# Optimization experiments

Measured on AMD Instinct MI355X. Metric: run time of the kernel, lower is better.

## Reference

```python
import jax, jax.numpy as jnp
import numpy as np

BS, NV, D, DFF, E, H = 32, 512, 128, 512, 8, 8
EPS = 1e-5

def layernorm(x, g, b):
    m = x.mean(-1, keepdims=True)
    v = ((x - m) ** 2).mean(-1, keepdims=True)
    return (x - m) / jnp.sqrt(v + EPS) * g + b

def setup_inputs() -> dict:
    key = jax.random.key(0)
    ks = jax.random.split(key, 10)
    s = lambda k, shape: (jax.random.normal(k, shape, jnp.float32) * 0.02)
    return {
        "x": jax.random.normal(ks[0], (BS, NV, D), jnp.float32),
        "cls_emd": jax.random.normal(ks[1], (E, D), jnp.float32),
        "Wq": s(ks[2], (D, D)), "Wk": s(ks[3], (D, D)),
        "Wv": s(ks[4], (D, D)), "Wo": s(ks[5], (D, D)),
        "Wg": s(ks[6], (D, D)),
        "W1": s(ks[7], (E, DFF, 2 * D)), "b1": jnp.zeros((E, DFF), jnp.float32),
        "W2": s(ks[8], (E, D, DFF)), "b2": jnp.zeros((E, D), jnp.float32),
        "g1": jnp.ones((D,), jnp.float32), "be1": jnp.zeros((D,), jnp.float32),
        "g2": jnp.ones((D,), jnp.float32), "be2": jnp.zeros((D,), jnp.float32),
    }

def reference(x, cls_emd, Wq, Wk, Wv, Wo, Wg, W1, b1, W2, b2, g1, be1, g2, be2):
    bs, n, d = x.shape
    dh = d // H
    # --- full multi-head self-attention over the variate axis ---
    q = (x @ Wq).reshape(bs, n, H, dh)
    k = (x @ Wk).reshape(bs, n, H, dh)
    v = (x @ Wv).reshape(bs, n, H, dh)
    scores = jnp.einsum('bnhd,bmhd->bhnm', q, k) * (1.0 / np.sqrt(dh))
    attn = jax.nn.softmax(scores, axis=-1)            # [bs, H, n, n]
    new_x = jnp.einsum('bhnm,bmhd->bnhd', attn, v).reshape(bs, n, d) @ Wo
    # residual + norm1 (dropout = identity in eval)
    x = layernorm(x + new_x, g1, be1)
    # --- gating: per-variate scores over clusters [n_vars, n_clusters] ---
    gate_scores = jax.nn.softmax((x.mean(0) @ Wg) @ cls_emd.T, axis=-1)
    # --- MoE: expand tokens vs every cluster, concat, per-cluster expert MLP ---
    ncl = cls_emd.shape[0]
    y = jnp.broadcast_to(x[:, :, None, :], (bs, n, ncl, d))
    z = jnp.broadcast_to(cls_emd[None, None, :, :], (bs, n, ncl, d))
    yz_cat = jnp.concatenate([y, z], axis=-1)          # [bs, n, K, 2d]
    h = jax.nn.relu(jnp.einsum('bnkc,kfc->bnkf', yz_cat, W1) + b1)  # kernel_size=1 conv == matmul
    expert_out = jnp.einsum('bnkf,kdf->bnkd', h, W2) + b2           # [bs, n, K, d]
    y_r = jnp.einsum('nk,bnkd->bnd', gate_scores, expert_out)
    out = layernorm(x + y_r, g2, be2)
    return (out, attn, gate_scores)
```

## Files before the change

kernel.cpp:

```cpp
#include <hip/hip_runtime.h>
#include <hip/hip_bf16.h>
#include <math.h>

#define BS   32
#define NV   512
#define D    128
#define DFF  512
#define E    8
#define NH   8
#define DH   16
#define M_TOK (BS*NV)
#define EPS  1e-5f

typedef __hip_bfloat16 bf16;
typedef _Float16 f16;
using sh8   = __attribute__((ext_vector_type(8))) short;
using us4   = __attribute__((ext_vector_type(4))) unsigned short;
using h4    = __attribute__((ext_vector_type(4))) _Float16;
using h8    = __attribute__((ext_vector_type(8))) _Float16;
using f32x4 = __attribute__((ext_vector_type(4))) float;

__device__ __forceinline__ float b2f(bf16 v){ return __bfloat162float(v); }
__device__ __forceinline__ bf16  f2b(float v){ return __float2bfloat16(v); }
__device__ __forceinline__ unsigned short f2bu(float v){
    bf16 b = __float2bfloat16(v);
    return __builtin_bit_cast(unsigned short, b);
}

__device__ __forceinline__ void gload_lds16(const void* g, void* l){
    __builtin_amdgcn_global_load_lds(
        (const __attribute__((address_space(1))) unsigned int*)g,
        (__attribute__((address_space(3))) unsigned int*)l, 16, 0, 0);
}

#define PR0 4096
#define PR1 (PR0 + 262144)
#define PR2 (PR1 + 131072)
#define PR3 (PR2 + 524288)
#define PR4 (PR3 + 49152)
#define PR5 (PR4 + 16384)
#define PREP_ITEMS PR5
__global__ __launch_bounds__(256) void k_prep(
    const float* __restrict__ W1, const float* __restrict__ W2,
    const float* __restrict__ x,  const float* __restrict__ Wq,
    const float* __restrict__ Wk, const float* __restrict__ Wv,
    const float* __restrict__ Wo, const float* __restrict__ b1,
    const float* __restrict__ cls,
    bf16* __restrict__ W1b, bf16* __restrict__ W2b, f16* __restrict__ xh,
    f16* __restrict__ WTq, f16* __restrict__ WoT, float* __restrict__ b1eff)
{
    int tid = blockIdx.x*256 + threadIdx.x;
    if (tid < PR0){
        int e = tid >> 9, f = tid & 511;
        float acc = b1[e*DFF + f];
        const float* wrow = W1 + ((size_t)e*DFF + f)*(2*D) + D;
        #pragma unroll 8
        for (int c=0;c<D;++c) acc += cls[e*D+c] * wrow[c];
        b1eff[tid] = acc;
    } else if (tid < PR1){
        int i = (tid - PR0)*4;
        float4 vv = *(const float4*)(W1 + i);
        us4 o; o[0]=f2bu(vv.x); o[1]=f2bu(vv.y); o[2]=f2bu(vv.z); o[3]=f2bu(vv.w);
        *(us4*)(W1b + i) = o;
    } else if (tid < PR2){
        int i = (tid - PR1)*4;
        float4 vv = *(const float4*)(W2 + i);
        us4 o; o[0]=f2bu(vv.x); o[1]=f2bu(vv.y); o[2]=f2bu(vv.z); o[3]=f2bu(vv.w);
        *(us4*)(W2b + i) = o;
    } else if (tid < PR3){
        int i = (tid - PR2)*4;
        float4 vv = *(const float4*)(x + i);
        h4 o; o[0]=(f16)vv.x; o[1]=(f16)vv.y; o[2]=(f16)vv.z; o[3]=(f16)vv.w;
        *(h4*)(xh + i) = o;
    } else if (tid < PR4){
        int idx = tid - PR3;
        int c = idx>>7, kk = idx&127;
        int which = c>>7, col = c&127;
        const float* W = which==0?Wq:(which==1?Wk:Wv);
        WTq[idx] = (f16)W[kk*D + col];
    } else if (tid < PR5){
        int idx = tid - PR4;
        int c = idx>>7, kk = idx&127;
        WoT[idx] = (f16)Wo[kk*D + c];
    }
}

__global__ __launch_bounds__(512) void k_qkv_mfma(
    const f16* __restrict__ xh, const f16* __restrict__ WT,
    f16* __restrict__ q, f16* __restrict__ k, f16* __restrict__ v)
{
    __shared__ __align__(16) char smem[65536];
    char* Xl = smem;
    char* Wl = smem + 16384;
    int t = threadIdx.x;
    int w = t>>6, lane = t&63;
    int bm = blockIdx.x, nh = blockIdx.y;

    const f16* xsrc = xh + (size_t)bm*64*D;
    #pragma unroll
    for (int i=0;i<2;++i){
        int ci = i*512 + t;
        int row = ci>>4, c16 = (ci&15)^(row&7);
        gload_lds16(xsrc + row*D + c16*8, Xl + (size_t)(i*512 + w*64)*16);
    }
    const f16* wsrc = WT + (size_t)nh*192*D;
    #pragma unroll
    for (int i=0;i<6;++i){
        int ci = i*512 + t;
        int row = ci>>4, c16 = (ci&15)^(row&7);
        gload_lds16(wsrc + row*D + c16*8, Wl + (size_t)(i*512 + w*64)*16);
    }
    __syncthreads();

    int rblk = w>>1, ch = w&1;
    int rl = lane&15, g = lane>>4;

    h8 afr[4];
    #pragma unroll
    for (int kk=0;kk<4;++kk){
        int row = rblk*16 + rl;
        int bo = (row<<8) + (kk<<6) + (g<<4); bo ^= (row&7)<<4;
        afr[kk] = *(const h8*)(Xl + bo);
    }
    f32x4 acc[6];
    #pragma unroll
    for (int nt=0;nt<6;++nt) acc[nt] = (f32x4){0.f,0.f,0.f,0.f};
    #pragma unroll
    for (int nt=0; nt<6; ++nt){
        #pragma unroll
        for (int kk=0;kk<4;++kk){
            int row = ch*96 + nt*16 + rl;
            int bo = (row<<8)+(kk<<6)+(g<<4); bo ^= (row&7)<<4;
            h8 bfr = *(const h8*)(Wl + bo);
            acc[nt] = __builtin_amdgcn_mfma_f32_16x16x32_f16(afr[kk], bfr, acc[nt],0,0,0);
        }
    }
    #pragma unroll
    for (int nt=0;nt<6;++nt){
        int cidx = nh*192 + ch*96 + nt*16 + rl;
        int which = cidx>>7, hh=(cidx>>4)&7, d = cidx&15;
        f16* dst = which==0?q:(which==1?k:v);
        #pragma unroll
        for (int j=0;j<4;++j){
            int m = bm*64 + rblk*16 + g*4 + j;
            int b = m>>9, n = m&511;
            dst[(((size_t)(b*NH+hh))*NV + n)*DH + d] = (f16)acc[nt][j];
        }
    }
}

#define KSTRIDE 24
#define VSTRIDE 520
#define PSTRIDE 68
__global__ __launch_bounds__(256) void k_attn2(
    const f16* __restrict__ q, const f16* __restrict__ kin, const f16* __restrict__ vin,
    float* __restrict__ attn_out, f16* __restrict__ ctx)
{
    __shared__ f16  Kl[512*KSTRIDE];
    __shared__ f16  VT[16*VSTRIDE];
    __shared__ f16  pbh[4][16*PSTRIDE];

    int bh = blockIdx.x;
    int t  = threadIdx.x;
    const f16* kb = kin + (size_t)bh*NV*DH;
    const f16* vb = vin + (size_t)bh*NV*DH;

    {
        int r0 = t*2;
        #pragma unroll
        for (int rr=0; rr<2; ++rr){
            const uint4* src = (const uint4*)(kb + (size_t)(r0+rr)*DH);
            *((uint4*)(Kl + (r0+rr)*KSTRIDE))     = src[0];
            *((uint4*)(Kl + (r0+rr)*KSTRIDE + 8)) = src[1];
        }
        const unsigned short* v0s = (const unsigned short*)(vb + (size_t)r0*DH);
        const unsigned short* v1s = v0s + DH;
        #pragma unroll
        for (int d=0; d<DH; ++d){
            unsigned u = (unsigned)v0s[d] | ((unsigned)v1s[d] << 16);
            *((unsigned*)(VT + d*VSTRIDE + r0)) = u;
        }
    }
    __syncthreads();

    int wave = t >> 6, lane = t & 63;
    int ql = lane & 15, g = lane >> 4;
    int q0 = blockIdx.y*64 + wave*16;

    h4 qf = *(const h4*)(q + ((size_t)bh*NV + q0 + ql)*DH + 4*g);
    #pragma unroll
    for (int i=0;i<4;++i) qf[i] = qf[i] * (_Float16)0.36067376f;

    f32x4 S[32];
    #pragma unroll
    for (int tt=0; tt<32; ++tt){
        h4 kf = *(const h4*)(Kl + (tt*16 + ql)*KSTRIDE + 4*g);
        S[tt] = __builtin_amdgcn_mfma_f32_16x16x16f16(kf, qf, (f32x4){0.f,0.f,0.f,0.f}, 0,0,0);
    }

    float sum = 0.f;
    #pragma unroll
    for (int tt=0; tt<32; ++tt)
        #pragma unroll
        for (int j=0;j<4;++j){
            float p = exp2f(S[tt][j]);
            S[tt][j] = p; sum += p;
        }
    sum += __shfl_xor(sum, 16);
    sum += __shfl_xor(sum, 32);
    float inv = 1.f/sum;
    #pragma unroll
    for (int tt=0; tt<32; ++tt)
        #pragma unroll
        for (int j=0;j<4;++j) S[tt][j] *= inv;

    f32x4 o0 = (f32x4){0.f,0.f,0.f,0.f}, o1 = (f32x4){0.f,0.f,0.f,0.f};
    f16* pw = pbh[wave];
    float* attnbase = attn_out + ((size_t)bh*NV + q0)*NV;
    int col16 = lane & 15, qg = lane >> 4;
    #pragma unroll
    for (int c=0; c<8; ++c){
        #pragma unroll
        for (int tt2=0; tt2<4; ++tt2){
            int tt = c*4 + tt2;
            h4 pf;
            pf[0]=(f16)S[tt][0]; pf[1]=(f16)S[tt][1];
            pf[2]=(f16)S[tt][2]; pf[3]=(f16)S[tt][3];
            h4 vf = *(const h4*)(VT + ql*VSTRIDE + tt*16 + 4*g);
            if (tt&1) o1 = __builtin_amdgcn_mfma_f32_16x16x16f16(vf, pf, o1, 0,0,0);
            else      o0 = __builtin_amdgcn_mfma_f32_16x16x16f16(vf, pf, o0, 0,0,0);
            *(h4*)(pw + ql*PSTRIDE + tt2*16 + 4*g) = pf;
        }
        asm volatile("" ::: "memory");
        #pragma unroll
        for (int rr=0; rr<4; ++rr){
            int qq = rr*4 + qg;
            h4 hv = *(const h4*)(pw + qq*PSTRIDE + col16*4);
            f32x4 vv;
            vv[0]=(float)hv[0]; vv[1]=(float)hv[1];
            vv[2]=(float)hv[2]; vv[3]=(float)hv[3];
            __builtin_nontemporal_store(vv, (f32x4*)(attnbase + (size_t)qq*NV + c*64 + col16*4));
        }
        asm volatile("" ::: "memory");
    }
    f32x4 o = o0 + o1;
    int b = bh >> 3, h = bh & 7;
    f16* cb = ctx + ((size_t)(b*NV) + q0 + ql)*D + h*DH + 4*g;
    h4 oc; oc[0]=(f16)o[0]; oc[1]=(f16)o[1]; oc[2]=(f16)o[2]; oc[3]=(f16)o[3];
    *(h4*)cb = oc;
}

__global__ __launch_bounds__(512) void k_woln_mfma(
    const f16* __restrict__ ctx, const f16* __restrict__ WoT,
    const float* __restrict__ x, const float* __restrict__ g1, const float* __restrict__ be1,
    bf16* __restrict__ x1b, float* __restrict__ yacc)
{
    __shared__ __align__(16) char smem[49152];
    __shared__ float lnred[2][64][2];
    char* Cl = smem;
    char* Wl = smem + 16384;
    int t = threadIdx.x;
    int w = t>>6, lane = t&63;
    int bm = blockIdx.x;

    const f16* csrc = ctx + (size_t)bm*64*D;
    #pragma unroll
    for (int i=0;i<2;++i){
        int ci = i*512 + t;
        int row = ci>>4, c16 = (ci&15)^(row&7);
        gload_lds16(csrc + row*D + c16*8, Cl + (size_t)(i*512 + w*64)*16);
    }
    #pragma unroll
    for (int i=0;i<4;++i){
        int ci = i*512 + t;
        int row = ci>>4, c16 = (ci&15)^(row&7);
        gload_lds16(WoT + row*D + c16*8, Wl + (size_t)(i*512 + w*64)*16);
    }
    __syncthreads();

    int rblk = w>>1, ch = w&1;
    int rl = lane&15, g = lane>>4;

    h8 afr[4];
    #pragma unroll
    for (int kk=0;kk<4;++kk){
        int row = rblk*16 + rl;
        int bo = (row<<8) + (kk<<6) + (g<<4); bo ^= (row&7)<<4;
        afr[kk] = *(const h8*)(Cl + bo);
    }
    f32x4 acc[4];
    #pragma unroll
    for (int nt=0;nt<4;++nt) acc[nt] = (f32x4){0.f,0.f,0.f,0.f};
    #pragma unroll
    for (int nt=0; nt<4; ++nt){
        #pragma unroll
        for (int kk=0;kk<4;++kk){
            int row = ch*64 + nt*16 + rl;
            int bo = (row<<8)+(kk<<6)+(g<<4); bo ^= (row&7)<<4;
            h8 bfr = *(const h8*)(Wl + bo);
            acc[nt] = __builtin_amdgcn_mfma_f32_16x16x32_f16(afr[kk], bfr, acc[nt],0,0,0);
        }
    }

    float rowv[4][4];
    #pragma unroll
    for (int j=0;j<4;++j){
        int m = bm*64 + rblk*16 + g*4 + j;
        #pragma unroll
        for (int dt=0;dt<4;++dt){
            int d = ch*64 + dt*16 + rl;
            rowv[j][dt] = acc[dt][j] + x[(size_t)m*D + d];
        }
    }
    #pragma unroll
    for (int j=0;j<4;++j){
        float s  = rowv[j][0]+rowv[j][1]+rowv[j][2]+rowv[j][3];
        float s2 = rowv[j][0]*rowv[j][0]+rowv[j][1]*rowv[j][1]
                 + rowv[j][2]*rowv[j][2]+rowv[j][3]*rowv[j][3];
        #pragma unroll
        for (int o=1;o<16;o<<=1){ s += __shfl_xor(s,o); s2 += __shfl_xor(s2,o); }
        if (rl==0){
            int row = rblk*16 + g*4 + j;
            lnred[ch][row][0] = s;
            lnred[ch][row][1] = s2;
        }
    }
    __syncthreads();
    #pragma unroll
    for (int j=0;j<4;++j){
        int row = rblk*16 + g*4 + j;
        float S  = lnred[0][row][0] + lnred[1][row][0];
        float S2 = lnred[0][row][1] + lnred[1][row][1];
        float mean = S*(1.f/D);
        float var  = S2*(1.f/D) - mean*mean;
        float rs = rsqrtf(var + EPS);
        int m = bm*64 + row;
        #pragma unroll
        for (int dt=0;dt<4;++dt){
            int d = ch*64 + dt*16 + rl;
            float o1 = (rowv[j][dt]-mean)*rs*g1[d] + be1[d];
            x1b[(size_t)m*D + d] = f2b(o1);
            yacc[(size_t)m*D + d] = o1;
        }
    }
}

__global__ __launch_bounds__(128) void k_gate(
    const float* __restrict__ yacc, const float* __restrict__ Wg, const float* __restrict__ cls,
    float* __restrict__ gate, float* __restrict__ gate_out)
{
    __shared__ float xm[D];
    __shared__ float tt[D];
    __shared__ float se[E];
    int n = blockIdx.x, t = threadIdx.x;
    float s = 0.f;
    #pragma unroll
    for (int b=0;b<BS;++b) s += yacc[((size_t)b*NV + n)*D + t];
    xm[t] = s * (1.f/BS);
    __syncthreads();
    float a = 0.f;
    for (int c=0;c<D;++c) a += xm[c] * Wg[c*D + t];
    tt[t] = a;
    __syncthreads();
    if (t < E){
        float acc=0.f;
        for (int c=0;c<D;++c) acc += tt[c] * cls[t*D + c];
        se[t]=acc;
    }
    __syncthreads();
    if (t==0){
        float mx=se[0];
        for(int e=1;e<E;++e) mx=fmaxf(mx,se[e]);
        float sm=0.f; float p[E];
        for(int e=0;e<E;++e){ p[e]=__expf(se[e]-mx); sm+=p[e]; }
        float inv=1.f/sm;
        for(int e=0;e<E;++e){
            gate[n*E+e]     = p[e]*inv;
            gate_out[n*E+e] = p[e]*inv;
        }
    }
}

__global__ __launch_bounds__(512) void k_moe_fused(
    const bf16* __restrict__ x1b, const bf16* __restrict__ W1b, const bf16* __restrict__ W2b,
    const float* __restrict__ b1eff, const float* __restrict__ b2,
    const float* __restrict__ gate, const float* __restrict__ yacc,
    const float* __restrict__ g2, const float* __restrict__ be2,
    float* __restrict__ out)
{
    __shared__ __align__(16) char smem[147456];
    char* Hl = smem + 131072;
    float (*lnred)[64][2] = (float (*)[64][2])Hl;

    int t = threadIdx.x;
    int w = t >> 6, lane = t & 63;
    int rblk = w >> 1, c = w & 1;
    int rl = lane & 15, g = lane >> 4;
    int bm = blockIdx.x;

    sh8 afr[4];
    {
        const bf16* Ab = x1b + (size_t)(bm*64 + rblk*16 + rl)*D;
        #pragma unroll
        for (int kk=0;kk<4;++kk) afr[kk] = *(const sh8*)(Ab + kk*32 + g*8);
    }

    f32x4 oacc[4];
    #pragma unroll
    for (int dt=0;dt<4;++dt) oacc[dt] = (f32x4){0.f,0.f,0.f,0.f};

    auto STAGE = [&](int idx, int buf){
        int e = idx >> 2, fc = idx & 3;
        const bf16* w1src = W1b + ((size_t)e*DFF + fc*128)*(2*D);
        const bf16* w2src = W2b + (size_t)e*D*DFF + fc*128;
        char* Wa = smem + buf*65536;
        char* Wb = Wa + 32768;
        #pragma unroll
        for (int i=0;i<4;++i){
            int ci  = (i*8 + w)*64 + lane;
            int row = ci >> 4;
            int c16 = (ci & 15) ^ (row & 7);
            gload_lds16(w1src + (size_t)row*256 + c16*8, Wa + (size_t)(i*8+w)*1024);
            gload_lds16(w2src + (size_t)row*512 + c16*8, Wb + (size_t)(i*8+w)*1024);
        }
    };

    STAGE(0, 0);
    asm volatile("s_waitcnt vmcnt(0)" ::: "memory");
    __syncthreads();

    f32x4 acc2e[4];
    #pragma unroll
    for (int dt=0;dt<4;++dt) acc2e[dt] = (f32x4){0.f,0.f,0.f,0.f};

    for (int idx=0; idx<32; ++idx){
        int buf = idx & 1;
        int e = idx >> 2, fc = idx & 3;
        char* Wa = smem + buf*65536;
        char* Wb = Wa + 32768;

        if (idx < 31) STAGE(idx+1, buf^1);

        f32x4 acc1[4];
        #pragma unroll
        for (int ft=0;ft<4;++ft) acc1[ft] = (f32x4){0.f,0.f,0.f,0.f};
        #pragma unroll
        for (int ft=0; ft<4; ++ft){
            int row = c*64 + ft*16 + rl;
            #pragma unroll
            for (int kk=0;kk<4;++kk){
                int bo = (row<<8) + (kk<<6) + (g<<4);
                bo ^= (row&7)<<4;
                sh8 bfr = *(const sh8*)(Wa + bo);
                acc1[ft] = __builtin_amdgcn_mfma_f32_16x16x32_bf16(afr[kk], bfr, acc1[ft], 0,0,0);
            }
        }
        #pragma unroll
        for (int ft=0; ft<4; ++ft){
            int fl = c*64 + ft*16 + rl;
            float bia = b1eff[e*DFF + fc*128 + fl];
            #pragma unroll
            for (int j=0;j<4;++j){
                int row = rblk*16 + g*4 + j;
                float v = acc1[ft][j] + bia;
                v = v > 0.f ? v : 0.f;
                int bo = (row<<8) + (fl<<1);
                bo ^= (row&7)<<4;
                *(bf16*)(Hl + bo) = f2b(v);
            }
        }
        __syncthreads();

        #pragma unroll
        for (int kk=0; kk<4; ++kk){
            int rowH = rblk*16 + rl;
            int boH = (rowH<<8) + (kk<<6) + (g<<4);
            boH ^= (rowH&7)<<4;
            sh8 hfr = *(const sh8*)(Hl + boH);
            #pragma unroll
            for (int dt=0;dt<4;++dt){
                int rowW = c*64 + dt*16 + rl;
                int boW = (rowW<<8) + (kk<<6) + (g<<4);
                boW ^= (rowW&7)<<4;
                sh8 bfr = *(const sh8*)(Wb + boW);
                acc2e[dt] = __builtin_amdgcn_mfma_f32_16x16x32_bf16(hfr, bfr, acc2e[dt], 0,0,0);
            }
        }

        if (fc == 3){
            #pragma unroll
            for (int j=0;j<4;++j){
                int m  = bm*64 + rblk*16 + g*4 + j;
                float gv = gate[(m & 511)*E + e];
                #pragma unroll
                for (int dt=0;dt<4;++dt){
                    int d = c*64 + dt*16 + rl;
                    oacc[dt][j] += gv*(acc2e[dt][j] + b2[e*D + d]);
                }
            }
            #pragma unroll
            for (int dt=0;dt<4;++dt) acc2e[dt] = (f32x4){0.f,0.f,0.f,0.f};
        }

        asm volatile("s_waitcnt vmcnt(0)" ::: "memory");
        __syncthreads();
    }

    float rowv[4][4];
    #pragma unroll
    for (int j=0;j<4;++j){
        int m = bm*64 + rblk*16 + g*4 + j;
        #pragma unroll
        for (int dt=0;dt<4;++dt){
            int d = c*64 + dt*16 + rl;
            rowv[j][dt] = oacc[dt][j] + yacc[(size_t)m*D + d];
        }
    }
    #pragma unroll
    for (int j=0;j<4;++j){
        float s  = rowv[j][0]+rowv[j][1]+rowv[j][2]+rowv[j][3];
        float s2 = rowv[j][0]*rowv[j][0]+rowv[j][1]*rowv[j][1]
                 + rowv[j][2]*rowv[j][2]+rowv[j][3]*rowv[j][3];
        #pragma unroll
        for (int o=1;o<16;o<<=1){ s += __shfl_xor(s,o); s2 += __shfl_xor(s2,o); }
        if (rl==0){
            int row = rblk*16 + g*4 + j;
            lnred[c][row][0] = s;
            lnred[c][row][1] = s2;
        }
    }
    __syncthreads();
    #pragma unroll
    for (int j=0;j<4;++j){
        int row = rblk*16 + g*4 + j;
        float S  = lnred[0][row][0] + lnred[1][row][0];
        float S2 = lnred[0][row][1] + lnred[1][row][1];
        float mean = S*(1.f/D);
        float var  = S2*(1.f/D) - mean*mean;
        float rs = rsqrtf(var + EPS);
        int m = bm*64 + row;
        #pragma unroll
        for (int dt=0;dt<4;++dt){
            int d = c*64 + dt*16 + rl;
            out[(size_t)m*D + d] = (rowv[j][dt]-mean)*rs*g2[d] + be2[d];
        }
    }
}

extern "C" void kernel_launch(void* const* d_in, const int* in_sizes, int n_in,
                              void* d_out, int out_size, void* d_ws, size_t ws_size,
                              hipStream_t stream)
{
    const float* x   = (const float*)d_in[0];
    const float* cls = (const float*)d_in[1];
    const float* Wq  = (const float*)d_in[2];
    const float* Wk  = (const float*)d_in[3];
    const float* Wv  = (const float*)d_in[4];
    const float* Wo  = (const float*)d_in[5];
    const float* Wg  = (const float*)d_in[6];
    const float* W1  = (const float*)d_in[7];
    const float* b1  = (const float*)d_in[8];
    const float* W2  = (const float*)d_in[9];
    const float* b2  = (const float*)d_in[10];
    const float* g1  = (const float*)d_in[11];
    const float* be1 = (const float*)d_in[12];
    const float* g2  = (const float*)d_in[13];
    const float* be2 = (const float*)d_in[14];

    float* out      = (float*)d_out;
    float* attn     = out + (size_t)M_TOK*D;
    float* gate_out = attn + (size_t)BS*NH*NV*NV;

    char* ws = (char*)d_ws;
    size_t off = 0;
    auto alloc = [&](size_t bytes)->void*{ void* p = ws + off; off += (bytes + 255) & ~(size_t)255; return p; };
    f16*   q    = (f16*)  alloc((size_t)M_TOK*D*2);
    f16*   kbuf = (f16*)  alloc((size_t)M_TOK*D*2);
    f16*   vbuf = (f16*)  alloc((size_t)M_TOK*D*2);
    f16*   ctx  = (f16*)  alloc((size_t)M_TOK*D*2);
    bf16*  x1b  = (bf16*) alloc((size_t)M_TOK*D*2);
    float* yacc = (float*)alloc((size_t)M_TOK*D*4);
    float* gate = (float*)alloc((size_t)NV*E*4);
    float* b1eff= (float*)alloc((size_t)E*DFF*4);
    bf16*  W1b  = (bf16*) alloc((size_t)E*DFF*2*D*2);
    bf16*  W2b  = (bf16*) alloc((size_t)E*D*DFF*2);
    f16*   xh   = (f16*)  alloc((size_t)M_TOK*D*2);
    f16*   WTq  = (f16*)  alloc((size_t)384*D*2);
    f16*   WoT  = (f16*)  alloc((size_t)D*D*2);

    k_prep<<<(PREP_ITEMS+255)/256, 256, 0, stream>>>(
        W1, W2, x, Wq, Wk, Wv, Wo, b1, cls,
        W1b, W2b, xh, WTq, WoT, b1eff);

    k_qkv_mfma<<<dim3(M_TOK/64, 2), 512, 0, stream>>>(xh, WTq, q, kbuf, vbuf);
    k_attn2<<<dim3(BS*NH, NV/64), 256, 0, stream>>>(q, kbuf, vbuf, attn, ctx);
    k_woln_mfma<<<M_TOK/64, 512, 0, stream>>>(ctx, WoT, x, g1, be1, x1b, yacc);
    k_gate<<<NV, 128, 0, stream>>>(yacc, Wg, cls, gate, gate_out);
    k_moe_fused<<<256, 512, 0, stream>>>(x1b, W1b, W2b, b1eff, b2, gate, yacc, g2, be2, out);
}
```

Measured before the change: 166.9 us.

## Switch fused MoE kernel to 32x32x16 MFMA with 2x4 warp tiling

Replaces the 16x16x32 bf16 MFMA tiling (each wave 16 rows x 64 cols) in the fused MoE kernel with 32x32x16 MFMAs, where each wave owns a 32x32 output tile in a 2x4 wave grid. The aim is to cut LDS fragment reads per MFMA and instruction count by reusing larger fragments. The bias/ReLU writeback, gate accumulation and final layernorm reduction are remapped to the 32x32 accumulator layout, with a 4-way cross-wave LN reduction. The cost is wider per-row shuffle reductions and different LDS bank access patterns.

Measured after the change: 165.7 us. No clear change (-0.7%).

```diff
diff --git a/kernel.cpp b/kernel.cpp
--- a/kernel.cpp
+++ b/kernel.cpp
@@ -19,6 +19,7 @@
 using h4    = __attribute__((ext_vector_type(4))) _Float16;
 using h8    = __attribute__((ext_vector_type(8))) _Float16;
 using f32x4 = __attribute__((ext_vector_type(4))) float;
+using f32x16 = __attribute__((ext_vector_type(16))) float;
 
 __device__ __forceinline__ float b2f(bf16 v){ return __bfloat162float(v); }
 __device__ __forceinline__ bf16  f2b(float v){ return __float2bfloat16(v); }
@@ -390,24 +391,23 @@
 {
     __shared__ __align__(16) char smem[147456];
     char* Hl = smem + 131072;
-    float (*lnred)[64][2] = (float (*)[64][2])Hl;
+    float (*lnred)[4][2] = (float (*)[4][2])Hl;
 
     int t = threadIdx.x;
     int w = t >> 6, lane = t & 63;
-    int rblk = w >> 1, c = w & 1;
-    int rl = lane & 15, g = lane >> 4;
+    int mb = w >> 2, nb = w & 3;
+    int l31 = lane & 31, h = lane >> 5;
     int bm = blockIdx.x;
 
-    sh8 afr[4];
+    sh8 afr[8];
     {
-        const bf16* Ab = x1b + (size_t)(bm*64 + rblk*16 + rl)*D;
-        #pragma unroll
-        for (int kk=0;kk<4;++kk) afr[kk] = *(const sh8*)(Ab + kk*32 + g*8);
-    }
-
-    f32x4 oacc[4];
-    #pragma unroll
-    for (int dt=0;dt<4;++dt) oacc[dt] = (f32x4){0.f,0.f,0.f,0.f};
+        const bf16* Ab = x1b + (size_t)(bm*64 + mb*32 + l31)*D;
+        #pragma unroll
+        for (int s=0;s<8;++s) afr[s] = *(const sh8*)(Ab + s*16 + h*8);
+    }
+
+    f32x16 oacc = {};
+    f32x16 acc2e = {};
 
     auto STAGE = [&](int idx, int buf){
         int e = idx >> 2, fc = idx & 3;
@@ -429,10 +429,6 @@
     asm volatile("s_waitcnt vmcnt(0)" ::: "memory");
     __syncthreads();
 
-    f32x4 acc2e[4];
-    #pragma unroll
-    for (int dt=0;dt<4;++dt) acc2e[dt] = (f32x4){0.f,0.f,0.f,0.f};
-
     for (int idx=0; idx<32; ++idx){
         int buf = idx & 1;
         int e = idx >> 2, fc = idx & 3;
@@ -441,109 +437,90 @@
 
         if (idx < 31) STAGE(idx+1, buf^1);
 
-        f32x4 acc1[4];
-        #pragma unroll
-        for (int ft=0;ft<4;++ft) acc1[ft] = (f32x4){0.f,0.f,0.f,0.f};
-        #pragma unroll
-        for (int ft=0; ft<4; ++ft){
-            int row = c*64 + ft*16 + rl;
+        f32x16 acc1 = {};
+        {
+            int row = nb*32 + l31;
+            int rbase = (row<<8);
+            int swz = (row&7)<<4;
             #pragma unroll
-            for (int kk=0;kk<4;++kk){
-                int bo = (row<<8) + (kk<<6) + (g<<4);
-                bo ^= (row&7)<<4;
+            for (int s=0;s<8;++s){
+                int bo = (rbase + s*32 + h*16) ^ swz;
                 sh8 bfr = *(const sh8*)(Wa + bo);
-                acc1[ft] = __builtin_amdgcn_mfma_f32_16x16x32_bf16(afr[kk], bfr, acc1[ft], 0,0,0);
+                acc1 = __builtin_amdgcn_mfma_f32_32x32x16_bf16(afr[s], bfr, acc1, 0,0,0);
             }
         }
-        #pragma unroll
-        for (int ft=0; ft<4; ++ft){
-            int fl = c*64 + ft*16 + rl;
-            float bia = b1eff[e*DFF + fc*128 + fl];
+        {
+            float bia = b1eff[e*DFF + fc*128 + nb*32 + l31];
             #pragma unroll
-            for (int j=0;j<4;++j){
-                int row = rblk*16 + g*4 + j;
-                float v = acc1[ft][j] + bia;
+            for (int r=0;r<16;++r){
+                int rowm = mb*32 + (r&3) + 8*(r>>2) + 4*h;
+                float v = acc1[r] + bia;
                 v = v > 0.f ? v : 0.f;
-                int bo = (row<<8) + (fl<<1);
-                bo ^= (row&7)<<4;
+                int bo = (rowm<<8) + ((nb*32 + l31)<<1);
+                bo ^= (rowm&7)<<4;
                 *(bf16*)(Hl + bo) = f2b(v);
             }
         }
         __syncthreads();
 
-        #pragma unroll
-        for (int kk=0; kk<4; ++kk){
-            int rowH = rblk*16 + rl;
-            int boH = (rowH<<8) + (kk<<6) + (g<<4);
-            boH ^= (rowH&7)<<4;
-            sh8 hfr = *(const sh8*)(Hl + boH);
+        {
+            int rowh = mb*32 + l31;
+            int hbase = (rowh<<8), hswz = (rowh&7)<<4;
+            int roww = nb*32 + l31;
+            int wbase = (roww<<8), wswz = (roww&7)<<4;
             #pragma unroll
-            for (int dt=0;dt<4;++dt){
-                int rowW = c*64 + dt*16 + rl;
-                int boW = (rowW<<8) + (kk<<6) + (g<<4);
-                boW ^= (rowW&7)<<4;
-                sh8 bfr = *(const sh8*)(Wb + boW);
-                acc2e[dt] = __builtin_amdgcn_mfma_f32_16x16x32_bf16(hfr, bfr, acc2e[dt], 0,0,0);
+            for (int s=0;s<8;++s){
+                sh8 hfr = *(const sh8*)(Hl + ((hbase + s*32 + h*16) ^ hswz));
+                sh8 wfr = *(const sh8*)(Wb + ((wbase + s*32 + h*16) ^ wswz));
+                acc2e = __builtin_amdgcn_mfma_f32_32x32x16_bf16(hfr, wfr, acc2e, 0,0,0);
             }
         }
 
         if (fc == 3){
+            int d = nb*32 + l31;
+            float bia2 = b2[e*D + d];
             #pragma unroll
-            for (int j=0;j<4;++j){
-                int m  = bm*64 + rblk*16 + g*4 + j;
+            for (int r=0;r<16;++r){
+                int m = bm*64 + mb*32 + (r&3) + 8*(r>>2) + 4*h;
                 float gv = gate[(m & 511)*E + e];
-                #pragma unroll
-                for (int dt=0;dt<4;++dt){
-                    int d = c*64 + dt*16 + rl;
-                    oacc[dt][j] += gv*(acc2e[dt][j] + b2[e*D + d]);
-                }
+                oacc[r] += gv*(acc2e[r] + bia2);
             }
-            #pragma unroll
-            for (int dt=0;dt<4;++dt) acc2e[dt] = (f32x4){0.f,0.f,0.f,0.f};
+            acc2e = (f32x16){};
         }
 
         asm volatile("s_waitcnt vmcnt(0)" ::: "memory");
         __syncthreads();
     }
 
-    float rowv[4][4];
-    #pragma unroll
-    for (int j=0;j<4;++j){
-        int m = bm*64 + rblk*16 + g*4 + j;
-        #pragma unroll
-        for (int dt=0;dt<4;++dt){
-            int d = c*64 + dt*16 + rl;
-            rowv[j][dt] = oacc[dt][j] + yacc[(size_t)m*D + d];
-        }
-    }
-    #pragma unroll
-    for (int j=0;j<4;++j){
-        float s  = rowv[j][0]+rowv[j][1]+rowv[j][2]+rowv[j][3];
-        float s2 = rowv[j][0]*rowv[j][0]+rowv[j][1]*rowv[j][1]
-                 + rowv[j][2]*rowv[j][2]+rowv[j][3]*rowv[j][3];
-        #pragma unroll
-        for (int o=1;o<16;o<<=1){ s += __shfl_xor(s,o); s2 += __shfl_xor(s2,o); }
-        if (rl==0){
-            int row = rblk*16 + g*4 + j;
-            lnred[c][row][0] = s;
-            lnred[c][row][1] = s2;
-        }
-    }
-    __syncthreads();
-    #pragma unroll
-    for (int j=0;j<4;++j){
-        int row = rblk*16 + g*4 + j;
-        float S  = lnred[0][row][0] + lnred[1][row][0];
-        float S2 = lnred[0][row][1] + lnred[1][row][1];
+    int d = nb*32 + l31;
+    float rowv[16];
+    #pragma unroll
+    for (int r=0;r<16;++r){
+        int m = bm*64 + mb*32 + (r&3) + 8*(r>>2) + 4*h;
+        rowv[r] = oacc[r] + yacc[(size_t)m*D + d];
+    }
+    #pragma unroll
+    for (int r=0;r<16;++r){
+        float s = rowv[r], s2 = rowv[r]*rowv[r];
+        #pragma unroll
+        for (int o=1;o<32;o<<=1){ s += __shfl_xor(s,o); s2 += __shfl_xor(s2,o); }
+        if (l31==0){
+            int rowl = mb*32 + (r&3) + 8*(r>>2) + 4*h;
+            lnred[rowl][nb][0] = s;
+            lnred[rowl][nb][1] = s2;
+        }
+    }
+    __syncthreads();
+    #pragma unroll
+    for (int r=0;r<16;++r){
+        int rowl = mb*32 + (r&3) + 8*(r>>2) + 4*h;
+        float S  = lnred[rowl][0][0]+lnred[rowl][1][0]+lnred[rowl][2][0]+lnred[rowl][3][0];
+        float S2 = lnred[rowl][0][1]+lnred[rowl][1][1]+lnred[rowl][2][1]+lnred[rowl][3][1];
         float mean = S*(1.f/D);
         float var  = S2*(1.f/D) - mean*mean;
         float rs = rsqrtf(var + EPS);
-        int m = bm*64 + row;
-        #pragma unroll
-        for (int dt=0;dt<4;++dt){
-            int d = c*64 + dt*16 + rl;
-            out[(size_t)m*D + d] = (rowv[j][dt]-mean)*rs*g2[d] + be2[d];
-        }
+        int m = bm*64 + rowl;
+        out[(size_t)m*D + d] = (rowv[r]-mean)*rs*g2[d] + be2[d];
     }
 }
 
```
